# Kernel tuning notes

Hardware: AMD Instinct MI355X
Metric: run time of the kernel (lower is better)

## Reference

```python
import jax, jax.numpy as jnp
import numpy as np


def setup_inputs() -> dict:
    key = jax.random.key(0)
    kx, ky = jax.random.split(key)
    B, N, M, D = 8, 4096, 4096, 128
    x = jax.random.normal(kx, (B, N, D), dtype=jnp.float32)
    y = jax.random.normal(ky, (B, M, D), dtype=jnp.float32)
    return {"x": x, "y": y}


def reference(x, y):
    # Pairwise L2 distances, equivalent to torch.cdist(x, y) (p=2).
    # ||x_i - y_j||^2 = ||x_i||^2 + ||y_j||^2 - 2 <x_i, y_j>
    x2 = jnp.sum(x * x, axis=-1)[:, :, None]          # [B, N, 1]
    y2 = jnp.sum(y * y, axis=-1)[:, None, :]          # [B, 1, M]
    xy = jnp.einsum("bnd,bmd->bnm", x, y)             # [B, N, M]
    D = jnp.sqrt(jnp.maximum(x2 + y2 - 2.0 * xy, 0.0))  # [B, N, M]
    coverage = D.min(axis=1).mean(axis=-1)            # min over N -> [B, M] -> [B]
    precision = D.min(axis=2).mean(axis=-1)           # min over M -> [B, N] -> [B]
    return (coverage + precision).mean()              # scalar Chamfer loss
```

## Files before the change

### kernel.cpp

```cpp
#include <hip/hip_runtime.h>
#include <cstdint>


#define B_   8
#define N_   4096
#define M_   4096
#define D_   128
#define TPB  8
#define ROWS_PB 512
#define XG   (N_ / ROWS_PB)
#define CHUNKS (M_ / (TPB * 64))

typedef __bf16 bf16x8 __attribute__((ext_vector_type(8)));
typedef float  f32x4  __attribute__((ext_vector_type(4)));
typedef unsigned int u32;

static __device__ __forceinline__ unsigned short f2bf(float f) {
  unsigned u = __float_as_uint(f);
  u += 0x7FFFu + ((u >> 16) & 1u);
  return (unsigned short)(u >> 16);
}

static __device__ __forceinline__ void gld16(void* lds, const void* g) {
  __builtin_amdgcn_global_load_lds(
      (const __attribute__((address_space(1))) void*)g,
      (__attribute__((address_space(3))) void*)lds, 16, 0, 0);
}

__global__ __launch_bounds__(256) void pass1_prep(
    const float* __restrict__ x, const float* __restrict__ y,
    unsigned short* __restrict__ xb, unsigned short* __restrict__ yb,
    float* __restrict__ x2, float* __restrict__ y2)
{
  const int ROWS = B_ * N_;
  int gw   = (blockIdx.x * 256 + threadIdx.x) >> 6;
  int lane = threadIdx.x & 63;
  int half = lane >> 5, sub = lane & 31;
  int row2 = gw * 2 + half;
  bool isx = row2 < ROWS;
  const float* src; unsigned short* dst; float* nrm; int row;
  if (isx) { src = x; dst = xb; nrm = x2; row = row2; }
  else     { src = y; dst = yb; nrm = y2; row = row2 - ROWS; }
  size_t base = (size_t)row * D_ + sub * 4;
  float4 v = *(const float4*)(src + base);
  float sx = isx ? -2.0f : 1.0f;
  u32 p0 = (u32)f2bf(sx * v.x) | ((u32)f2bf(sx * v.y) << 16);
  u32 p1 = (u32)f2bf(sx * v.z) | ((u32)f2bf(sx * v.w) << 16);
  *(uint2*)(dst + base) = make_uint2(p0, p1);
  float s = v.x * v.x + v.y * v.y + v.z * v.z + v.w * v.w;
  #pragma unroll
  for (int m = 1; m < 32; m <<= 1) s += __shfl_xor(s, m, 64);
  if (sub == 0) nrm[row] = s;
}

__global__
__launch_bounds__(512)
__attribute__((amdgpu_waves_per_eu(2)))
void pass2_tile(
    const unsigned short* __restrict__ xb, const unsigned short* __restrict__ yb,
    const float* __restrict__ x2, const float* __restrict__ y2,
    float* __restrict__ rowpart, float* __restrict__ colpart)
{
  __shared__ unsigned short ys[2 * 8192];
  __shared__ float cminW[2][8 * 64];
  __shared__ float y2s[TPB * 64];

  const int tid  = threadIdx.x;
  const int wave = tid >> 6;
  const int lane = tid & 63;
  const int quad = lane >> 4;
  const int l15  = lane & 15;

  const int id    = blockIdx.x;
  const int b     = id & 7;
  const int j     = id >> 3;
  const int xg    = j & 7;
  const int chunk = j >> 3;
  const int n0    = xg * ROWS_PB;
  const int mc0   = chunk * (TPB * 64);

  int srcoff[2], ldsoff[2];
  #pragma unroll
  for (int i = 0; i < 2; ++i) {
    int p  = (wave * 2 + i) * 1024 + lane * 16;
    int r  = p >> 8;
    int pc = (p >> 4) & 15;
    int c  = pc ^ (r & 15);
    srcoff[i] = r * D_ + c * 8;
    ldsoff[i] = (wave * 2 + i) * 1024;
  }

  {
    const unsigned short* src = yb + ((size_t)b * M_ + mc0) * D_;
    gld16((char*)ys + ldsoff[0], src + srcoff[0]);
    gld16((char*)ys + ldsoff[1], src + srcoff[1]);
  }
  if (tid < TPB * 64) y2s[tid] = y2[(size_t)b * M_ + mc0 + tid];

  bf16x8 afrag[4][4];
  const size_t xrow0 = (size_t)b * N_ + n0 + wave * 64;
  #pragma unroll
  for (int kb = 0; kb < 4; ++kb)
    #pragma unroll
    for (int rt = 0; rt < 4; ++rt)
      afrag[kb][rt] = *(const bf16x8*)(xb + (xrow0 + rt * 16 + l15) * D_ + kb * 32 + quad * 8);

  float xv[4][4];
  #pragma unroll
  for (int rt = 0; rt < 4; ++rt)
    #pragma unroll
    for (int r = 0; r < 4; ++r)
      xv[rt][r] = x2[(size_t)b * N_ + n0 + wave * 64 + rt * 16 + quad * 4 + r];

  const float FINF = __uint_as_float(0x7F800000u);
  float rmin2[4][4];
  #pragma unroll
  for (int rt = 0; rt < 4; ++rt)
    #pragma unroll
    for (int r = 0; r < 4; ++r) rmin2[rt][r] = FINF;

  #pragma unroll 1
  for (int t = 0; t < TPB; ++t) {
    const int m0 = mc0 + t * 64;
    const int d  = (t & 1) * 16384;
    __syncthreads();

    if (t + 1 < TPB) {
      const unsigned short* src = yb + ((size_t)b * M_ + m0 + 64) * D_;
      char* dst = (char*)ys + (16384 - d);
      gld16(dst + ldsoff[0], src + srcoff[0]);
      gld16(dst + ldsoff[1], src + srcoff[1]);
    }

    if (t > 0 && tid < 64) {
      float v = cminW[(t - 1) & 1][tid];
      #pragma unroll
      for (int w = 1; w < 8; ++w) v = fminf(v, cminW[(t - 1) & 1][w * 64 + tid]);
      colpart[(size_t)xg * (B_ * M_) + (size_t)b * M_ + (m0 - 64) + tid] = v;
    }

    #pragma unroll
    for (int ct = 0; ct < 4; ++ct) {
      f32x4 a[4];
      #pragma unroll
      for (int rt = 0; rt < 4; ++rt) a[rt] = (f32x4)(0.0f);
      #pragma unroll
      for (int kb = 0; kb < 4; ++kb) {
        const int row = ct * 16 + l15;
        const int pcB = (kb * 4 + quad) ^ l15;
        bf16x8 bfr = *(const bf16x8*)((const char*)ys + d + row * 256 + pcB * 16);
        #pragma unroll
        for (int rt = 0; rt < 4; ++rt)
          a[rt] = __builtin_amdgcn_mfma_f32_16x16x32_bf16(afrag[kb][rt], bfr, a[rt], 0, 0, 0);
      }
      float yv = y2s[t * 64 + ct * 16 + l15];
      float cm = FINF;
      #pragma unroll
      for (int rt = 0; rt < 4; ++rt) {
        #pragma unroll
        for (int r = 0; r < 4; ++r) {
          float s = a[rt][r] + xv[rt][r] + yv;
          rmin2[rt][r] = fminf(rmin2[rt][r], s);
          cm = fminf(cm, s);
        }
      }
      cm = fminf(cm, __shfl_xor(cm, 16, 64));
      cm = fminf(cm, __shfl_xor(cm, 32, 64));
      if (lane < 16) cminW[t & 1][wave * 64 + ct * 16 + lane] = cm;
    }
  }

  __syncthreads();
  if (tid < 64) {
    float v = cminW[(TPB - 1) & 1][tid];
    #pragma unroll
    for (int w = 1; w < 8; ++w) v = fminf(v, cminW[(TPB - 1) & 1][w * 64 + tid]);
    colpart[(size_t)xg * (B_ * M_) + (size_t)b * M_ + (mc0 + (TPB - 1) * 64) + tid] = v;
  }

  #pragma unroll
  for (int rt = 0; rt < 4; ++rt) {
    #pragma unroll
    for (int r = 0; r < 4; ++r) {
      float v = rmin2[rt][r];
      v = fminf(v, __shfl_xor(v, 1, 64));
      v = fminf(v, __shfl_xor(v, 2, 64));
      v = fminf(v, __shfl_xor(v, 4, 64));
      v = fminf(v, __shfl_xor(v, 8, 64));
      if (l15 == 0)
        rowpart[(size_t)chunk * (B_ * N_) + (size_t)b * N_ + n0 + wave * 64 + rt * 16 + quad * 4 + r] = v;
    }
  }
}

__global__ __launch_bounds__(256) void pass3_partial(
    const float* __restrict__ rowpart, const float* __restrict__ colpart,
    float* __restrict__ partial)
{
  const int BN = B_ * N_;
  float s1 = 0.0f, s2 = 0.0f;
  for (int i = blockIdx.x * 256 + threadIdx.x; i < BN; i += 64 * 256) {
    float r = rowpart[i];
    #pragma unroll
    for (int c = 1; c < CHUNKS; ++c) r = fminf(r, rowpart[c * BN + i]);
    s1 += sqrtf(fmaxf(r, 0.0f));
    float m = colpart[i];
    #pragma unroll
    for (int g = 1; g < XG; ++g) m = fminf(m, colpart[g * BN + i]);
    s2 += sqrtf(fmaxf(m, 0.0f));
  }
  #pragma unroll
  for (int m = 1; m < 64; m <<= 1) { s1 += __shfl_xor(s1, m, 64); s2 += __shfl_xor(s2, m, 64); }
  __shared__ float r1[4], r2[4];
  int wave = threadIdx.x >> 6, lane = threadIdx.x & 63;
  if (lane == 0) { r1[wave] = s1; r2[wave] = s2; }
  __syncthreads();
  if (threadIdx.x == 0) {
    partial[blockIdx.x]      = r1[0] + r1[1] + r1[2] + r1[3];
    partial[64 + blockIdx.x] = r2[0] + r2[1] + r2[2] + r2[3];
  }
}

__global__ void pass4_final(const float* __restrict__ partial, float* __restrict__ out)
{
  int lane = threadIdx.x;
  float s = partial[lane] + partial[64 + lane];
  #pragma unroll
  for (int m = 1; m < 64; m <<= 1) s += __shfl_xor(s, m, 64);
  if (lane == 0) out[0] = s / (float)(B_ * N_);
}

extern "C" void kernel_launch(void* const* d_in, const int* in_sizes, int n_in,
                              void* d_out, int out_size, void* d_ws, size_t ws_size,
                              hipStream_t stream)
{
  const float* x = (const float*)d_in[0];
  const float* y = (const float*)d_in[1];
  char* ws = (char*)d_ws;

  unsigned short* xb = (unsigned short*)(ws);
  unsigned short* yb = (unsigned short*)(ws + (8u << 20));
  float* x2      = (float*)(ws + (16u << 20));
  float* y2      = (float*)(ws + (16u << 20) + (1u << 17));
  float* rowpart = (float*)(ws + (16u << 20) + (2u << 17));
  float* colpart = (float*)(ws + (16u << 20) + (10u << 17));
  float* partial = (float*)(ws + (16u << 20) + (18u << 17));
  float* outf = (float*)d_out;

  pass1_prep<<<(B_ * N_) / 4, 256, 0, stream>>>(x, y, xb, yb, x2, y2);

  pass2_tile<<<B_ * XG * CHUNKS, 512, 0, stream>>>(xb, yb, x2, y2, rowpart, colpart);

  pass3_partial<<<64, 256, 0, stream>>>(rowpart, colpart, partial);
  pass4_final<<<1, 64, 0, stream>>>(partial, outf);
}
```

Baseline: 128.6 us.

## Fold x-norm into MFMA accumulator, drop column shuffles, fuse final reduction via atomics

The MFMA accumulators are now initialized with the x-norm vector, which removes one add per element in the epilogue. The cross-quad shuffle reduction of column minima is replaced by writing all 32 per-quad partials to a larger LDS buffer, which the leader threads reduce over 32 entries. The last two reduction kernels are merged into one that atomically adds into the output after a memset, saving one launch. The waves_per_eu hint is also removed, which may change register allocation and occupancy, and the larger LDS footprint may limit occupancy as well.

```diff
diff --git a/kernel.cpp b/kernel.cpp
--- a/kernel.cpp
+++ b/kernel.cpp
@@ -53,16 +53,13 @@
   if (sub == 0) nrm[row] = s;
 }
 
-__global__
-__launch_bounds__(512)
-__attribute__((amdgpu_waves_per_eu(2)))
-void pass2_tile(
+__global__ __launch_bounds__(512) void pass2_tile(
     const unsigned short* __restrict__ xb, const unsigned short* __restrict__ yb,
     const float* __restrict__ x2, const float* __restrict__ y2,
     float* __restrict__ rowpart, float* __restrict__ colpart)
 {
   __shared__ unsigned short ys[2 * 8192];
-  __shared__ float cminW[2][8 * 64];
+  __shared__ float cminW[2][32 * 64];
   __shared__ float y2s[TPB * 64];
 
   const int tid  = threadIdx.x;
@@ -105,12 +102,12 @@
     for (int rt = 0; rt < 4; ++rt)
       afrag[kb][rt] = *(const bf16x8*)(xb + (xrow0 + rt * 16 + l15) * D_ + kb * 32 + quad * 8);
 
-  float xv[4][4];
+  f32x4 xvv[4];
   #pragma unroll
   for (int rt = 0; rt < 4; ++rt)
     #pragma unroll
     for (int r = 0; r < 4; ++r)
-      xv[rt][r] = x2[(size_t)b * N_ + n0 + wave * 64 + rt * 16 + quad * 4 + r];
+      xvv[rt][r] = x2[(size_t)b * N_ + n0 + wave * 64 + rt * 16 + quad * 4 + r];
 
   const float FINF = __uint_as_float(0x7F800000u);
   float rmin2[4][4];
@@ -133,9 +130,10 @@
     }
 
     if (t > 0 && tid < 64) {
-      float v = cminW[(t - 1) & 1][tid];
-      #pragma unroll
-      for (int w = 1; w < 8; ++w) v = fminf(v, cminW[(t - 1) & 1][w * 64 + tid]);
+      const float* cb = cminW[(t - 1) & 1];
+      float v = cb[tid];
+      #pragma unroll
+      for (int w = 1; w < 32; ++w) v = fminf(v, cb[w * 64 + tid]);
       colpart[(size_t)xg * (B_ * M_) + (size_t)b * M_ + (m0 - 64) + tid] = v;
     }
 
@@ -143,7 +141,7 @@
     for (int ct = 0; ct < 4; ++ct) {
       f32x4 a[4];
       #pragma unroll
-      for (int rt = 0; rt < 4; ++rt) a[rt] = (f32x4)(0.0f);
+      for (int rt = 0; rt < 4; ++rt) a[rt] = xvv[rt];
       #pragma unroll
       for (int kb = 0; kb < 4; ++kb) {
         const int row = ct * 16 + l15;
@@ -159,22 +157,21 @@
       for (int rt = 0; rt < 4; ++rt) {
         #pragma unroll
         for (int r = 0; r < 4; ++r) {
-          float s = a[rt][r] + xv[rt][r] + yv;
+          float s = a[rt][r] + yv;
           rmin2[rt][r] = fminf(rmin2[rt][r], s);
           cm = fminf(cm, s);
         }
       }
-      cm = fminf(cm, __shfl_xor(cm, 16, 64));
-      cm = fminf(cm, __shfl_xor(cm, 32, 64));
-      if (lane < 16) cminW[t & 1][wave * 64 + ct * 16 + lane] = cm;
+      cminW[t & 1][(wave * 4 + quad) * 64 + ct * 16 + l15] = cm;
     }
   }
 
   __syncthreads();
   if (tid < 64) {
-    float v = cminW[(TPB - 1) & 1][tid];
-    #pragma unroll
-    for (int w = 1; w < 8; ++w) v = fminf(v, cminW[(TPB - 1) & 1][w * 64 + tid]);
+    const float* cb = cminW[(TPB - 1) & 1];
+    float v = cb[tid];
+    #pragma unroll
+    for (int w = 1; w < 32; ++w) v = fminf(v, cb[w * 64 + tid]);
     colpart[(size_t)xg * (B_ * M_) + (size_t)b * M_ + (mc0 + (TPB - 1) * 64) + tid] = v;
   }
 
@@ -193,9 +190,9 @@
   }
 }
 
-__global__ __launch_bounds__(256) void pass3_partial(
+__global__ __launch_bounds__(256) void pass3_final(
     const float* __restrict__ rowpart, const float* __restrict__ colpart,
-    float* __restrict__ partial)
+    float* __restrict__ out)
 {
   const int BN = B_ * N_;
   float s1 = 0.0f, s2 = 0.0f;
@@ -209,25 +206,15 @@
     for (int g = 1; g < XG; ++g) m = fminf(m, colpart[g * BN + i]);
     s2 += sqrtf(fmaxf(m, 0.0f));
   }
-  #pragma unroll
-  for (int m = 1; m < 64; m <<= 1) { s1 += __shfl_xor(s1, m, 64); s2 += __shfl_xor(s2, m, 64); }
-  __shared__ float r1[4], r2[4];
+  float s = s1 + s2;
+  #pragma unroll
+  for (int m = 1; m < 64; m <<= 1) s += __shfl_xor(s, m, 64);
+  __shared__ float r1[4];
   int wave = threadIdx.x >> 6, lane = threadIdx.x & 63;
-  if (lane == 0) { r1[wave] = s1; r2[wave] = s2; }
+  if (lane == 0) r1[wave] = s;
   __syncthreads();
-  if (threadIdx.x == 0) {
-    partial[blockIdx.x]      = r1[0] + r1[1] + r1[2] + r1[3];
-    partial[64 + blockIdx.x] = r2[0] + r2[1] + r2[2] + r2[3];
-  }
-}
-
-__global__ void pass4_final(const float* __restrict__ partial, float* __restrict__ out)
-{
-  int lane = threadIdx.x;
-  float s = partial[lane] + partial[64 + lane];
-  #pragma unroll
-  for (int m = 1; m < 64; m <<= 1) s += __shfl_xor(s, m, 64);
-  if (lane == 0) out[0] = s / (float)(B_ * N_);
+  if (threadIdx.x == 0)
+    atomicAdd(out, (r1[0] + r1[1] + r1[2] + r1[3]) / (float)(B_ * N_));
 }
 
 extern "C" void kernel_launch(void* const* d_in, const int* in_sizes, int n_in,
@@ -244,13 +231,13 @@
   float* y2      = (float*)(ws + (16u << 20) + (1u << 17));
   float* rowpart = (float*)(ws + (16u << 20) + (2u << 17));
   float* colpart = (float*)(ws + (16u << 20) + (10u << 17));
-  float* partial = (float*)(ws + (16u << 20) + (18u << 17));
   float* outf = (float*)d_out;
 
+  hipMemsetAsync(outf, 0, sizeof(float), stream);
+
   pass1_prep<<<(B_ * N_) / 4, 256, 0, stream>>>(x, y, xb, yb, x2, y2);
 
   pass2_tile<<<B_ * XG * CHUNKS, 512, 0, stream>>>(xb, yb, x2, y2, rowpart, colpart);
 
-  pass3_partial<<<64, 256, 0, stream>>>(rowpart, colpart, partial);
-  pass4_final<<<1, 64, 0, stream>>>(partial, outf);
-}
+  pass3_final<<<64, 256, 0, stream>>>(rowpart, colpart, outf);
+}
```

Result: faster. 121.6 us (-5.4%).
